# Kernel tuning notes

Hardware: AMD Instinct MI355X
Metric: run time of the kernel (lower is better)

Reference implementation:

```python
import jax, jax.numpy as jnp
import numpy as np

L = 8            # hash grid levels
T = 2 ** 19      # table size per level
F = 4            # feature dims per level
H = 64           # hidden features
BASE_RES, MAX_RES = 16.0, 1024.0
RES = jnp.asarray(BASE_RES * (MAX_RES / BASE_RES) ** (np.arange(L) / (L - 1)), dtype=jnp.float32)
PRIMES = jnp.array([1, 2654435761, 805459861], dtype=jnp.uint32)
CORNERS = jnp.array([[i >> 2 & 1, i >> 1 & 1, i & 1] for i in range(8)], dtype=jnp.float32)  # [8,3]
CORNERS_U = CORNERS.astype(jnp.uint32)


def hash_grid_encode(points, tables):
    # points: [N,3] in [0,1]; tables: [L,T,F] -> [N, L*F]
    def level(table, res):
        p = points * res                       # [N,3]
        p0 = jnp.floor(p)
        frac = p - p0                          # [N,3]
        idx0 = p0.astype(jnp.uint32)
        cidx = idx0[:, None, :] + CORNERS_U[None]          # [N,8,3]
        h = cidx * PRIMES                                   # uint32 wraparound
        h = (h[..., 0] ^ h[..., 1] ^ h[..., 2]) % jnp.uint32(T)
        feats = table[h.astype(jnp.int32)]                  # [N,8,F]
        w = jnp.prod(jnp.where(CORNERS[None] == 1.0, frac[:, None, :], 1.0 - frac[:, None, :]), axis=-1)  # [N,8]
        return jnp.sum(feats * w[..., None], axis=1)        # [N,F]
    out = jax.vmap(level, in_axes=(0, 0))(tables, RES)      # [L,N,F]
    return jnp.transpose(out, (1, 0, 2)).reshape(points.shape[0], L * F)


def sh4_encode(d):
    # 4th order (16-component) spherical harmonics of unit directions
    d = d / jnp.linalg.norm(d, axis=-1, keepdims=True)
    x, y, z = d[..., 0], d[..., 1], d[..., 2]
    xx, yy, zz = x * x, y * y, z * z
    return jnp.stack([
        jnp.full_like(x, 0.28209479177387814),
        -0.48860251190291987 * y,
        0.48860251190291987 * z,
        -0.48860251190291987 * x,
        1.0925484305920792 * x * y,
        -1.0925484305920792 * y * z,
        0.94617469575755997 * zz - 0.31539156525252005,
        -1.0925484305920792 * x * z,
        0.54627421529603959 * (xx - yy),
        -0.59004358992664352 * y * (3.0 * xx - yy),
        2.8906114426405538 * x * y * z,
        -0.45704579946446572 * y * (4.0 * zz - xx - yy),
        0.37317633259011546 * z * (2.0 * zz - 3.0 * xx - 3.0 * yy),
        -0.45704579946446572 * x * (4.0 * zz - xx - yy),
        1.4453057213202769 * z * (xx - yy),
        -0.59004358992664352 * x * (xx - 3.0 * yy),
    ], axis=-1)


def _dense(key, fan_in, fan_out):
    kw, kb = jax.random.split(key)
    W = jax.random.normal(kw, (fan_in, fan_out), jnp.float32) / jnp.sqrt(fan_in)
    b = jnp.zeros((fan_out,), jnp.float32)
    return W, b


def setup_inputs() -> dict:
    key = jax.random.key(0)
    ks = jax.random.split(key, 10)
    N = 524288
    input_points = jax.random.uniform(ks[0], (N, 3), jnp.float32)
    input_views = jax.random.normal(ks[1], (N, 3), jnp.float32)
    tables = jax.random.uniform(ks[2], (L, T, F), jnp.float32, -1e-4, 1e-4)
    W1, b1 = _dense(ks[3], L * F, H)
    W2, b2 = _dense(ks[4], H, H)
    W3, b3 = _dense(ks[5], H, 16)
    W4, b4 = _dense(ks[6], 15 + 16, H)
    W5, b5 = _dense(ks[7], H, H)
    W6, b6 = _dense(ks[8], H, H)
    W7, b7 = _dense(ks[9], H, 3)
    return dict(input_points=input_points, input_views=input_views, tables=tables,
                W1=W1, b1=b1, W2=W2, b2=b2, W3=W3, b3=b3, W4=W4, b4=b4,
                W5=W5, b5=b5, W6=W6, b6=b6, W7=W7, b7=b7)


def reference(input_points, input_views, tables, W1, b1, W2, b2, W3, b3, W4, b4, W5, b5, W6, b6, W7, b7):
    enc = hash_grid_encode(input_points, tables)       # [N,32]
    x = jax.nn.relu(enc @ W1 + b1)
    x = jax.nn.relu(x @ W2 + b2)
    x = x @ W3 + b3                                    # [N,16]
    densities = jax.nn.relu(x[..., 0])
    enc_dir = sh4_encode(input_views)                  # [N,16]
    x = jnp.concatenate([x[..., 1:], enc_dir], axis=-1)  # [N,31]
    x = jax.nn.relu(x @ W4 + b4)
    x = jax.nn.relu(x @ W5 + b5)
    x = jax.nn.relu(x @ W6 + b6)
    x = x @ W7 + b7                                    # [N,3]
    colors = jax.nn.sigmoid(x)
    return colors, densities
```

## Files before the change

### kernel.cpp

```cpp
#include <hip/hip_runtime.h>
#include <math.h>

#define TSZ (1u << 19)
#define TMASK (TSZ - 1u)

typedef __attribute__((ext_vector_type(8))) short bf8_t;
typedef __attribute__((ext_vector_type(4))) float f32x4;
typedef _Float16 h2_t __attribute__((ext_vector_type(2)));

struct ResArr { float r[8]; };
struct WPtrs { const float* w[7]; };

__device__ __forceinline__ unsigned short f2b(float x) {
    unsigned u = __float_as_uint(x);
    return (unsigned short)((u + 0x7fffu + ((u >> 16) & 1u)) >> 16);
}
__device__ __forceinline__ unsigned pack2(float a, float b) {
    return (unsigned)f2b(a) | ((unsigned)f2b(b) << 16);
}

__device__ __forceinline__ int swadr(int row, int e) {
    return row * 128 + ((((e >> 3) ^ (row & 7)) << 4)) + ((e & 7) << 1);
}

__device__ __forceinline__ unsigned enc8(float x) {
    float v = x * 1048576.0f;
    unsigned u = __float_as_uint(v);
    unsigned s = (u >> 24) & 0x80u;
    unsigned ua = u & 0x7fffffffu;
    unsigned r = ua + 0x7ffffu + ((ua >> 20) & 1u);
    int E = (int)(r >> 23) - 120;
    unsigned nrm = ((unsigned)E << 3) | ((r >> 20) & 7u);
    float t = __uint_as_float(ua) * 512.0f + 12582912.0f;
    unsigned den = __float_as_uint(t) & 0xfu;
    unsigned mag = (__uint_as_float(ua) >= 0.015625f) ? nrm : den;
    return s | mag;
}

__global__ void prep_all(const float4* __restrict__ tbl, uint4* __restrict__ tab_out,
                         WPtrs wp, unsigned short* __restrict__ wfrag) {
    int b = blockIdx.x;
    if (b < 4096) {
        int i = b * 256 + threadIdx.x;
        uint4 o;
        { float4 v = tbl[4 * i + 0]; o.x = enc8(v.x) | (enc8(v.y) << 8) | (enc8(v.z) << 16) | (enc8(v.w) << 24); }
        { float4 v = tbl[4 * i + 1]; o.y = enc8(v.x) | (enc8(v.y) << 8) | (enc8(v.z) << 16) | (enc8(v.w) << 24); }
        { float4 v = tbl[4 * i + 2]; o.z = enc8(v.x) | (enc8(v.y) << 8) | (enc8(v.z) << 16) | (enc8(v.w) << 24); }
        { float4 v = tbl[4 * i + 3]; o.w = enc8(v.x) | (enc8(v.y) << 8) | (enc8(v.z) << 16) | (enc8(v.w) << 24); }
        tab_out[i] = o;
        return;
    }
    int idx = (b - 4096) * 256 + threadIdx.x;
    if (idx >= 18432) return;
    int layer, base;
    if      (idx < 2048)  { layer = 0; base = 0;     }
    else if (idx < 6144)  { layer = 1; base = 2048;  }
    else if (idx < 7168)  { layer = 2; base = 6144;  }
    else if (idx < 9216)  { layer = 3; base = 7168;  }
    else if (idx < 13312) { layer = 4; base = 9216;  }
    else if (idx < 17408) { layer = 5; base = 13312; }
    else                  { layer = 6; base = 17408; }
    int rel  = idx - base;
    int frag = rel >> 9;
    int r    = rel & 511;
    int lane = r >> 3, j = r & 7;
    int quad = lane >> 4, col16 = lane & 15;
    int KS = (layer == 0 || layer == 3) ? 1 : 2;
    int nt = frag / KS, ks = frag % KS;
    int k = ks * 32 + quad * 8 + j;
    int n = nt * 16 + col16;
    int Kreal = (layer == 0) ? 32 : (layer == 3) ? 31 : 64;
    int Nw    = (layer == 2) ? 16 : (layer == 6) ? 3  : 64;
    float v = 0.0f;
    if (k < Kreal && n < Nw) v = wp.w[layer][k * Nw + n];
    wfrag[idx] = f2b(v);
}

__global__ void __launch_bounds__(256, 2) ngp_mfma(
    const float* __restrict__ pts, const float* __restrict__ views,
    const unsigned* __restrict__ tab8,
    const unsigned short* __restrict__ wfrag,
    const float* __restrict__ b1, const float* __restrict__ b2,
    const float* __restrict__ b3, const float* __restrict__ b4,
    const float* __restrict__ b5, const float* __restrict__ b6,
    const float* __restrict__ b7,
    ResArr res, float* __restrict__ out_col, float* __restrict__ out_den,
    int npts)
{
    __shared__ unsigned char act[4][8192];
    const int tid   = threadIdx.x;
    const int w     = tid >> 6;
    const int lane  = tid & 63;
    const int quad  = lane >> 4;
    const int col16 = lane & 15;
    unsigned char* actb = act[w];

    const int n0 = blockIdx.x * 256 + w * 64;
    if (n0 >= npts) return;
    int pt = n0 + lane;
    int ptc = pt < npts ? pt : npts - 1;

    const float px = pts[3 * ptc + 0];
    const float py = pts[3 * ptc + 1];
    const float pz = pts[3 * ptc + 2];
    float vx = views[3 * ptc + 0], vy = views[3 * ptc + 1], vz = views[3 * ptc + 2];

    uint2    gp[8][4];
    unsigned gs[8][4] = {};
    unsigned meta[8];
    float    tfr[8][3];
#pragma unroll
    for (int l = 0; l < 8; ++l) {
        float rr = res.r[l];
        float fx = px * rr, fy = py * rr, fz = pz * rr;
        float f0x = floorf(fx), f0y = floorf(fy), f0z = floorf(fz);
        unsigned ix = (unsigned)f0x, iy = (unsigned)f0y, iz = (unsigned)f0z;
        tfr[l][0] = fx - f0x; tfr[l][1] = fy - f0y; tfr[l][2] = fz - f0z;
        unsigned hy  = iy * 2654435761u,  hz  = iz * 805459861u;
        unsigned hy1 = hy + 2654435761u,  hz1 = hz + 805459861u;
        unsigned syz[4] = { hy ^ hz, hy ^ hz1, hy1 ^ hz, hy1 ^ hz1 };
        const unsigned* tl = tab8 + (size_t)l * TSZ;
        unsigned m = (ix & 1u) << 4;
#pragma unroll
        for (int c = 0; c < 4; ++c) {
            unsigned h0 = (ix ^ syz[c]) & TMASK;
            gp[l][c] = ((const uint2*)tl)[h0 >> 1];
            m |= (h0 & 1u) << c;
        }
        meta[l] = m;
        if (ix & 1u) {
            unsigned x1 = ix + 1u;
#pragma unroll
            for (int c = 0; c < 4; ++c) {
                unsigned h1 = (x1 ^ syz[c]) & TMASK;
                gs[l][c] = tl[h1];
            }
        }
    }

    float4 stash;
#pragma unroll
    for (int l = 0; l < 8; ++l) {
        float tx = tfr[l][0], ty = tfr[l][1], tz = tfr[l][2];
        float wx1 = tx, wx0 = 1.0f - tx;
        float wy1 = ty, wy0 = 1.0f - ty;
        float wz1 = tz, wz0 = 1.0f - tz;
        float wyz[4] = { wy0 * wz0, wy0 * wz1, wy1 * wz0, wy1 * wz1 };
        unsigned m = meta[l];
        h2_t acc01 = { (_Float16)0, (_Float16)0 };
        h2_t acc23 = { (_Float16)0, (_Float16)0 };
#pragma unroll
        for (int c = 0; c < 4; ++c) {
            uint2 pr = gp[l][c];
            bool hodd = (m >> c) & 1u;
            unsigned mine = hodd ? pr.y : pr.x;
            unsigned oth  = hodd ? pr.x : pr.y;
            unsigned nxt  = (m & 16u) ? gs[l][c] : oth;
#pragma unroll
            for (int half = 0; half < 2; ++half) {
                float wt = (half ? wx1 : wx0) * wyz[c];
                unsigned u = half ? nxt : mine;
                unsigned ws = (unsigned)__builtin_bit_cast(unsigned short, (_Float16)wt);
                h2_t w2 = __builtin_bit_cast(h2_t, __builtin_amdgcn_perm(0u, ws, 0x01000100u));
                unsigned p01 = __builtin_amdgcn_perm(0u, u, 0x01040004u);
                unsigned p23 = __builtin_amdgcn_perm(0u, u, 0x03040204u);
                unsigned m01 = (((p01 >> 1) & 0x3F803F80u) + 0x20002000u) | (p01 & 0x80008000u);
                unsigned m23 = (((p23 >> 1) & 0x3F803F80u) + 0x20002000u) | (p23 & 0x80008000u);
                acc01 = __builtin_bit_cast(h2_t, m01) * w2 + acc01;
                acc23 = __builtin_bit_cast(h2_t, m23) * w2 + acc23;
            }
        }
        const float SC = 9.5367431640625e-07f;
        float a0 = (float)acc01[0] * SC, a1 = (float)acc01[1] * SC;
        float a2 = (float)acc23[0] * SC, a3 = (float)acc23[1] * SC;
        if ((l & 1) == 0) {
            stash = make_float4(a0, a1, a2, a3);
        } else {
            uint4 pk;
            pk.x = pack2(stash.x, stash.y);
            pk.y = pack2(stash.z, stash.w);
            pk.z = pack2(a0, a1);
            pk.w = pack2(a2, a3);
            *(uint4*)(actb + lane * 128 + ((((l >> 1)) ^ (lane & 7)) << 4)) = pk;
        }
    }

    float inv = rsqrtf(vx * vx + vy * vy + vz * vz);
    vx *= inv; vy *= inv; vz *= inv;
    float xx = vx * vx, yy = vy * vy, zz = vz * vz;
    float sh[16];
    sh[0]  = 0.28209479177387814f;
    sh[1]  = -0.48860251190291987f * vy;
    sh[2]  = 0.48860251190291987f * vz;
    sh[3]  = -0.48860251190291987f * vx;
    sh[4]  = 1.0925484305920792f * vx * vy;
    sh[5]  = -1.0925484305920792f * vy * vz;
    sh[6]  = 0.94617469575755997f * zz - 0.31539156525252005f;
    sh[7]  = -1.0925484305920792f * vx * vz;
    sh[8]  = 0.54627421529603959f * (xx - yy);
    sh[9]  = -0.59004358992664352f * vy * (3.0f * xx - yy);
    sh[10] = 2.8906114426405538f * vx * vy * vz;
    sh[11] = -0.45704579946446572f * vy * (4.0f * zz - xx - yy);
    sh[12] = 0.37317633259011546f * vz * (2.0f * zz - 3.0f * xx - 3.0f * yy);
    sh[13] = -0.45704579946446572f * vx * (4.0f * zz - xx - yy);
    sh[14] = 1.4453057213202769f * vz * (xx - yy);
    sh[15] = -0.59004358992664352f * vx * (xx - 3.0f * yy);

#define LAYER_STD(KS, FB, BIAS)                                                          \
    {                                                                                    \
        bf8_t A[4][KS];                                                                  \
        _Pragma("unroll") for (int mt = 0; mt < 4; ++mt)                                 \
            _Pragma("unroll") for (int ks = 0; ks < KS; ++ks)                            \
                A[mt][ks] = *(const bf8_t*)(actb + swadr(mt * 16 + col16, ks * 32 + quad * 8)); \
        _Pragma("unroll") for (int nt = 0; nt < 4; ++nt) {                               \
            float bv = BIAS[nt * 16 + col16];                                            \
            f32x4 acc[4];                                                                \
            _Pragma("unroll") for (int mt = 0; mt < 4; ++mt) acc[mt] = f32x4{bv, bv, bv, bv}; \
            _Pragma("unroll") for (int ks = 0; ks < KS; ++ks) {                          \
                bf8_t B = ((const bf8_t*)(wfrag + FB + (nt * KS + ks) * 512))[lane];     \
                _Pragma("unroll") for (int mt = 0; mt < 4; ++mt)                         \
                    acc[mt] = __builtin_amdgcn_mfma_f32_16x16x32_bf16(A[mt][ks], B, acc[mt], 0, 0, 0); \
            }                                                                            \
            _Pragma("unroll") for (int mt = 0; mt < 4; ++mt)                             \
                _Pragma("unroll") for (int r = 0; r < 4; ++r) {                          \
                    int row = mt * 16 + quad * 4 + r;                                    \
                    *(unsigned short*)(actb + swadr(row, nt * 16 + col16)) =             \
                        f2b(fmaxf(acc[mt][r], 0.0f));                                    \
                }                                                                        \
        }                                                                                \
    }

    LAYER_STD(1, 0, b1)
    LAYER_STD(2, 2048, b2)

    {
        bf8_t A[4][2];
#pragma unroll
        for (int mt = 0; mt < 4; ++mt)
#pragma unroll
            for (int ks = 0; ks < 2; ++ks)
                A[mt][ks] = *(const bf8_t*)(actb + swadr(mt * 16 + col16, ks * 32 + quad * 8));
        float bv = b3[col16];
        f32x4 acc[4];
#pragma unroll
        for (int mt = 0; mt < 4; ++mt) acc[mt] = f32x4{bv, bv, bv, bv};
#pragma unroll
        for (int ks = 0; ks < 2; ++ks) {
            bf8_t B = ((const bf8_t*)(wfrag + 6144 + ks * 512))[lane];
#pragma unroll
            for (int mt = 0; mt < 4; ++mt)
                acc[mt] = __builtin_amdgcn_mfma_f32_16x16x32_bf16(A[mt][ks], B, acc[mt], 0, 0, 0);
        }
#pragma unroll
        for (int mt = 0; mt < 4; ++mt)
#pragma unroll
            for (int r = 0; r < 4; ++r) {
                int row = mt * 16 + quad * 4 + r;
                float v = acc[mt][r];
                if (col16 == 0) {
                    if (n0 + row < npts) out_den[n0 + row] = fmaxf(v, 0.0f);
                } else {
                    *(unsigned short*)(actb + swadr(row, col16 - 1)) = f2b(v);
                }
            }
    }

#pragma unroll
    for (int i = 0; i < 16; ++i)
        *(unsigned short*)(actb + swadr(lane, 15 + i)) = f2b(sh[i]);
    *(unsigned short*)(actb + swadr(lane, 31)) = 0;

    LAYER_STD(1, 7168, b4)
    LAYER_STD(2, 9216, b5)
    LAYER_STD(2, 13312, b6)

    {
        bf8_t A[4][2];
#pragma unroll
        for (int mt = 0; mt < 4; ++mt)
#pragma unroll
            for (int ks = 0; ks < 2; ++ks)
                A[mt][ks] = *(const bf8_t*)(actb + swadr(mt * 16 + col16, ks * 32 + quad * 8));
        float bv = (col16 < 3) ? b7[col16] : 0.0f;
        f32x4 acc[4];
#pragma unroll
        for (int mt = 0; mt < 4; ++mt) acc[mt] = f32x4{bv, bv, bv, bv};
#pragma unroll
        for (int ks = 0; ks < 2; ++ks) {
            bf8_t B = ((const bf8_t*)(wfrag + 17408 + ks * 512))[lane];
#pragma unroll
            for (int mt = 0; mt < 4; ++mt)
                acc[mt] = __builtin_amdgcn_mfma_f32_16x16x32_bf16(A[mt][ks], B, acc[mt], 0, 0, 0);
        }
        if (col16 < 3) {
#pragma unroll
            for (int mt = 0; mt < 4; ++mt)
#pragma unroll
                for (int r = 0; r < 4; ++r) {
                    int row = mt * 16 + quad * 4 + r;
                    if (n0 + row < npts) {
                        float s = 1.0f / (1.0f + expf(-acc[mt][r]));
                        out_col[(size_t)(n0 + row) * 3 + col16] = s;
                    }
                }
        }
    }
#undef LAYER_STD
}

extern "C" void kernel_launch(void* const* d_in, const int* in_sizes, int n_in,
                              void* d_out, int out_size, void* d_ws, size_t ws_size,
                              hipStream_t stream) {
    const float* pts    = (const float*)d_in[0];
    const float* views  = (const float*)d_in[1];
    const float* tables = (const float*)d_in[2];
    const float* W1 = (const float*)d_in[3];  const float* b1 = (const float*)d_in[4];
    const float* W2 = (const float*)d_in[5];  const float* b2 = (const float*)d_in[6];
    const float* W3 = (const float*)d_in[7];  const float* b3 = (const float*)d_in[8];
    const float* W4 = (const float*)d_in[9];  const float* b4 = (const float*)d_in[10];
    const float* W5 = (const float*)d_in[11]; const float* b5 = (const float*)d_in[12];
    const float* W6 = (const float*)d_in[13]; const float* b6 = (const float*)d_in[14];
    const float* W7 = (const float*)d_in[15]; const float* b7 = (const float*)d_in[16];

    const int N = in_sizes[0] / 3;
    float* out = (float*)d_out;
    float* out_col = out;
    float* out_den = out + (size_t)3 * N;

    unsigned* tab8        = (unsigned*)d_ws;
    unsigned short* wfrag = (unsigned short*)((char*)d_ws + (size_t)(TSZ) * 8 * 4);

    WPtrs wp;
    wp.w[0] = W1; wp.w[1] = W2; wp.w[2] = W3; wp.w[3] = W4;
    wp.w[4] = W5; wp.w[5] = W6; wp.w[6] = W7;
    prep_all<<<4096 + 72, 256, 0, stream>>>((const float4*)tables, (uint4*)tab8, wp, wfrag);

    ResArr res;
    for (int l = 0; l < 8; ++l)
        res.r[l] = (float)(16.0 * pow(64.0, (double)l / 7.0));

    const int grid = (N + 255) / 256;
    ngp_mfma<<<grid, 256, 0, stream>>>(pts, views, tab8, wfrag,
                                       b1, b2, b3, b4, b5, b6, b7,
                                       res, out_col, out_den, N);
}
```

Measured before the change: 291.9 us.

## Pipeline hash-grid gathers through a three-level rolling buffer and raise occupancy

Replaces the issue-all-eight-levels-then-combine gather scheme with a three-slot rolling pipeline: gathers for the next levels are issued while the current level is interpolated, and sched_barriers keep that order. This cuts the live register footprint of the gather buffers, which lets launch bounds ask for three blocks per SM instead of two. Spherical-harmonic computation is also moved to the point of use so its registers are not live during the gather phase. The trade-off is fewer gathers in flight per wave, offset by more resident waves, and the scheduling barriers may limit the compiler's freedom to interleave work.

```diff
diff --git a/kernel.cpp b/kernel.cpp
--- a/kernel.cpp
+++ b/kernel.cpp
@@ -76,7 +76,7 @@
     wfrag[idx] = f2b(v);
 }
 
-__global__ void __launch_bounds__(256, 2) ngp_mfma(
+__global__ void __launch_bounds__(256, 3) ngp_mfma(
     const float* __restrict__ pts, const float* __restrict__ views,
     const unsigned* __restrict__ tab8,
     const unsigned short* __restrict__ wfrag,
@@ -105,106 +105,99 @@
     const float pz = pts[3 * ptc + 2];
     float vx = views[3 * ptc + 0], vy = views[3 * ptc + 1], vz = views[3 * ptc + 2];
 
-    uint2    gp[8][4];
-    unsigned gs[8][4] = {};
-    unsigned meta[8];
-    float    tfr[8][3];
-#pragma unroll
-    for (int l = 0; l < 8; ++l) {
-        float rr = res.r[l];
-        float fx = px * rr, fy = py * rr, fz = pz * rr;
-        float f0x = floorf(fx), f0y = floorf(fy), f0z = floorf(fz);
-        unsigned ix = (unsigned)f0x, iy = (unsigned)f0y, iz = (unsigned)f0z;
-        tfr[l][0] = fx - f0x; tfr[l][1] = fy - f0y; tfr[l][2] = fz - f0z;
-        unsigned hy  = iy * 2654435761u,  hz  = iz * 805459861u;
-        unsigned hy1 = hy + 2654435761u,  hz1 = hz + 805459861u;
-        unsigned syz[4] = { hy ^ hz, hy ^ hz1, hy1 ^ hz, hy1 ^ hz1 };
-        const unsigned* tl = tab8 + (size_t)l * TSZ;
-        unsigned m = (ix & 1u) << 4;
-#pragma unroll
-        for (int c = 0; c < 4; ++c) {
-            unsigned h0 = (ix ^ syz[c]) & TMASK;
-            gp[l][c] = ((const uint2*)tl)[h0 >> 1];
-            m |= (h0 & 1u) << c;
-        }
-        meta[l] = m;
-        if (ix & 1u) {
-            unsigned x1 = ix + 1u;
-#pragma unroll
-            for (int c = 0; c < 4; ++c) {
-                unsigned h1 = (x1 ^ syz[c]) & TMASK;
-                gs[l][c] = tl[h1];
-            }
-        }
-    }
-
-    float4 stash;
-#pragma unroll
-    for (int l = 0; l < 8; ++l) {
-        float tx = tfr[l][0], ty = tfr[l][1], tz = tfr[l][2];
-        float wx1 = tx, wx0 = 1.0f - tx;
-        float wy1 = ty, wy0 = 1.0f - ty;
-        float wz1 = tz, wz0 = 1.0f - tz;
-        float wyz[4] = { wy0 * wz0, wy0 * wz1, wy1 * wz0, wy1 * wz1 };
-        unsigned m = meta[l];
-        h2_t acc01 = { (_Float16)0, (_Float16)0 };
-        h2_t acc23 = { (_Float16)0, (_Float16)0 };
-#pragma unroll
-        for (int c = 0; c < 4; ++c) {
-            uint2 pr = gp[l][c];
-            bool hodd = (m >> c) & 1u;
-            unsigned mine = hodd ? pr.y : pr.x;
-            unsigned oth  = hodd ? pr.x : pr.y;
-            unsigned nxt  = (m & 16u) ? gs[l][c] : oth;
-#pragma unroll
-            for (int half = 0; half < 2; ++half) {
-                float wt = (half ? wx1 : wx0) * wyz[c];
-                unsigned u = half ? nxt : mine;
-                unsigned ws = (unsigned)__builtin_bit_cast(unsigned short, (_Float16)wt);
-                h2_t w2 = __builtin_bit_cast(h2_t, __builtin_amdgcn_perm(0u, ws, 0x01000100u));
-                unsigned p01 = __builtin_amdgcn_perm(0u, u, 0x01040004u);
-                unsigned p23 = __builtin_amdgcn_perm(0u, u, 0x03040204u);
-                unsigned m01 = (((p01 >> 1) & 0x3F803F80u) + 0x20002000u) | (p01 & 0x80008000u);
-                unsigned m23 = (((p23 >> 1) & 0x3F803F80u) + 0x20002000u) | (p23 & 0x80008000u);
-                acc01 = __builtin_bit_cast(h2_t, m01) * w2 + acc01;
-                acc23 = __builtin_bit_cast(h2_t, m23) * w2 + acc23;
-            }
-        }
-        const float SC = 9.5367431640625e-07f;
-        float a0 = (float)acc01[0] * SC, a1 = (float)acc01[1] * SC;
-        float a2 = (float)acc23[0] * SC, a3 = (float)acc23[1] * SC;
-        if ((l & 1) == 0) {
-            stash = make_float4(a0, a1, a2, a3);
-        } else {
-            uint4 pk;
-            pk.x = pack2(stash.x, stash.y);
-            pk.y = pack2(stash.z, stash.w);
-            pk.z = pack2(a0, a1);
-            pk.w = pack2(a2, a3);
-            *(uint4*)(actb + lane * 128 + ((((l >> 1)) ^ (lane & 7)) << 4)) = pk;
-        }
-    }
-
-    float inv = rsqrtf(vx * vx + vy * vy + vz * vz);
-    vx *= inv; vy *= inv; vz *= inv;
-    float xx = vx * vx, yy = vy * vy, zz = vz * vz;
-    float sh[16];
-    sh[0]  = 0.28209479177387814f;
-    sh[1]  = -0.48860251190291987f * vy;
-    sh[2]  = 0.48860251190291987f * vz;
-    sh[3]  = -0.48860251190291987f * vx;
-    sh[4]  = 1.0925484305920792f * vx * vy;
-    sh[5]  = -1.0925484305920792f * vy * vz;
-    sh[6]  = 0.94617469575755997f * zz - 0.31539156525252005f;
-    sh[7]  = -1.0925484305920792f * vx * vz;
-    sh[8]  = 0.54627421529603959f * (xx - yy);
-    sh[9]  = -0.59004358992664352f * vy * (3.0f * xx - yy);
-    sh[10] = 2.8906114426405538f * vx * vy * vz;
-    sh[11] = -0.45704579946446572f * vy * (4.0f * zz - xx - yy);
-    sh[12] = 0.37317633259011546f * vz * (2.0f * zz - 3.0f * xx - 3.0f * yy);
-    sh[13] = -0.45704579946446572f * vx * (4.0f * zz - xx - yy);
-    sh[14] = 1.4453057213202769f * vz * (xx - yy);
-    sh[15] = -0.59004358992664352f * vx * (xx - 3.0f * yy);
+    uint2    gp[3][4];
+    unsigned gs[3][4];
+    unsigned meta[3];
+    float    tf[3][3];
+    float4   stash;
+
+#define GI(l, s) { \
+    float rr = res.r[l]; \
+    float fx = px * rr, fy = py * rr, fz = pz * rr; \
+    float f0x = floorf(fx), f0y = floorf(fy), f0z = floorf(fz); \
+    unsigned ix = (unsigned)f0x, iy = (unsigned)f0y, iz = (unsigned)f0z; \
+    tf[s][0] = fx - f0x; tf[s][1] = fy - f0y; tf[s][2] = fz - f0z; \
+    unsigned hy  = iy * 2654435761u,  hz  = iz * 805459861u; \
+    unsigned hy1 = hy + 2654435761u,  hz1 = hz + 805459861u; \
+    unsigned syz0 = hy ^ hz, syz1 = hy ^ hz1, syz2 = hy1 ^ hz, syz3 = hy1 ^ hz1; \
+    const unsigned* tl = tab8 + (size_t)(l) * TSZ; \
+    unsigned mm = (ix & 1u) << 4; \
+    { unsigned h0 = (ix ^ syz0) & TMASK; gp[s][0] = ((const uint2*)tl)[h0 >> 1]; mm |= (h0 & 1u); } \
+    { unsigned h0 = (ix ^ syz1) & TMASK; gp[s][1] = ((const uint2*)tl)[h0 >> 1]; mm |= (h0 & 1u) << 1; } \
+    { unsigned h0 = (ix ^ syz2) & TMASK; gp[s][2] = ((const uint2*)tl)[h0 >> 1]; mm |= (h0 & 1u) << 2; } \
+    { unsigned h0 = (ix ^ syz3) & TMASK; gp[s][3] = ((const uint2*)tl)[h0 >> 1]; mm |= (h0 & 1u) << 3; } \
+    meta[s] = mm; \
+    if (ix & 1u) { \
+        unsigned x1 = ix + 1u; \
+        gs[s][0] = tl[(x1 ^ syz0) & TMASK]; \
+        gs[s][1] = tl[(x1 ^ syz1) & TMASK]; \
+        gs[s][2] = tl[(x1 ^ syz2) & TMASK]; \
+        gs[s][3] = tl[(x1 ^ syz3) & TMASK]; \
+    } \
+}
+
+#define HALF(u_, wt_) { \
+    float wt = (wt_); unsigned u = (u_); \
+    unsigned ws = (unsigned)__builtin_bit_cast(unsigned short, (_Float16)wt); \
+    h2_t w2 = __builtin_bit_cast(h2_t, __builtin_amdgcn_perm(0u, ws, 0x01000100u)); \
+    unsigned p01 = __builtin_amdgcn_perm(0u, u, 0x01040004u); \
+    unsigned p23 = __builtin_amdgcn_perm(0u, u, 0x03040204u); \
+    unsigned m01 = (((p01 >> 1) & 0x3F803F80u) + 0x20002000u) | (p01 & 0x80008000u); \
+    unsigned m23 = (((p23 >> 1) & 0x3F803F80u) + 0x20002000u) | (p23 & 0x80008000u); \
+    acc01 = __builtin_bit_cast(h2_t, m01) * w2 + acc01; \
+    acc23 = __builtin_bit_cast(h2_t, m23) * w2 + acc23; \
+}
+
+#define CORNER(s, c, wyzc) { \
+    uint2 pr = gp[s][c]; \
+    bool hodd = (mc >> (c)) & 1u; \
+    unsigned mine = hodd ? pr.y : pr.x; \
+    unsigned oth  = hodd ? pr.x : pr.y; \
+    unsigned nxt  = (mc & 16u) ? gs[s][c] : oth; \
+    HALF(mine, wx0 * (wyzc)) \
+    HALF(nxt,  wx1 * (wyzc)) \
+}
+
+#define GC(l, s) { \
+    float tx = tf[s][0], ty = tf[s][1], tz = tf[s][2]; \
+    float wx1 = tx, wx0 = 1.0f - tx; \
+    float wy1 = ty, wy0 = 1.0f - ty; \
+    float wz1 = tz, wz0 = 1.0f - tz; \
+    float wyz0 = wy0 * wz0, wyz1 = wy0 * wz1, wyz2 = wy1 * wz0, wyz3 = wy1 * wz1; \
+    unsigned mc = meta[s]; \
+    h2_t acc01 = { (_Float16)0, (_Float16)0 }; \
+    h2_t acc23 = { (_Float16)0, (_Float16)0 }; \
+    CORNER(s, 0, wyz0) CORNER(s, 1, wyz1) CORNER(s, 2, wyz2) CORNER(s, 3, wyz3) \
+    const float SC = 9.5367431640625e-07f;   \
+    float a0 = (float)acc01[0] * SC, a1 = (float)acc01[1] * SC; \
+    float a2 = (float)acc23[0] * SC, a3 = (float)acc23[1] * SC; \
+    if (((l) & 1) == 0) { \
+        stash = make_float4(a0, a1, a2, a3); \
+    } else { \
+        uint4 pk_; \
+        pk_.x = pack2(stash.x, stash.y); \
+        pk_.y = pack2(stash.z, stash.w); \
+        pk_.z = pack2(a0, a1); \
+        pk_.w = pack2(a2, a3); \
+        *(uint4*)(actb + lane * 128 + (((((l) >> 1)) ^ (lane & 7)) << 4)) = pk_; \
+    } \
+}
+
+    GI(0, 0) GI(1, 1) GI(2, 2)
+    __builtin_amdgcn_sched_barrier(0);
+    GC(0, 0) GI(3, 0) __builtin_amdgcn_sched_barrier(0);
+    GC(1, 1) GI(4, 1) __builtin_amdgcn_sched_barrier(0);
+    GC(2, 2) GI(5, 2) __builtin_amdgcn_sched_barrier(0);
+    GC(3, 0) GI(6, 0) __builtin_amdgcn_sched_barrier(0);
+    GC(4, 1) GI(7, 1) __builtin_amdgcn_sched_barrier(0);
+    GC(5, 2)
+    GC(6, 0)
+    GC(7, 1)
+
+#undef GC
+#undef CORNER
+#undef HALF
+#undef GI
 
 #define LAYER_STD(KS, FB, BIAS)                                                          \
     {                                                                                    \
@@ -265,10 +258,33 @@
             }
     }
 
-#pragma unroll
-    for (int i = 0; i < 16; ++i)
-        *(unsigned short*)(actb + swadr(lane, 15 + i)) = f2b(sh[i]);
-    *(unsigned short*)(actb + swadr(lane, 31)) = 0;
+    {
+        float inv = rsqrtf(vx * vx + vy * vy + vz * vz);
+        vx *= inv; vy *= inv; vz *= inv;
+        float xx = vx * vx, yy = vy * vy, zz = vz * vz;
+        float sh[16];
+        sh[0]  = 0.28209479177387814f;
+        sh[1]  = -0.48860251190291987f * vy;
+        sh[2]  = 0.48860251190291987f * vz;
+        sh[3]  = -0.48860251190291987f * vx;
+        sh[4]  = 1.0925484305920792f * vx * vy;
+        sh[5]  = -1.0925484305920792f * vy * vz;
+        sh[6]  = 0.94617469575755997f * zz - 0.31539156525252005f;
+        sh[7]  = -1.0925484305920792f * vx * vz;
+        sh[8]  = 0.54627421529603959f * (xx - yy);
+        sh[9]  = -0.59004358992664352f * vy * (3.0f * xx - yy);
+        sh[10] = 2.8906114426405538f * vx * vy * vz;
+        sh[11] = -0.45704579946446572f * vy * (4.0f * zz - xx - yy);
+        sh[12] = 0.37317633259011546f * vz * (2.0f * zz - 3.0f * xx - 3.0f * yy);
+        sh[13] = -0.45704579946446572f * vx * (4.0f * zz - xx - yy);
+        sh[14] = 1.4453057213202769f * vz * (xx - yy);
+        sh[15] = -0.59004358992664352f * vx * (xx - 3.0f * yy);
+
+#pragma unroll
+        for (int i = 0; i < 16; ++i)
+            *(unsigned short*)(actb + swadr(lane, 15 + i)) = f2b(sh[i]);
+        *(unsigned short*)(actb + swadr(lane, 31)) = 0;
+    }
 
     LAYER_STD(1, 7168, b4)
     LAYER_STD(2, 9216, b5)
```

Measured after the change: 277.4 us. 1.05x faster.

## Split hash-grid gather into a separate per-level kernel before the MLP

Applied to the files above, without the earlier changes.

Splits the fused kernel in two. A new kernel runs one block per 256 points per level, gathers the table entries, trilerps them, and writes packed bf16 features to a workspace buffer. The MLP kernel then reads those features, computes the SH encoding later to shorten register live ranges, and runs at higher occupancy (launch bound raised from 2 to 4 blocks). This trades a global round trip for the encoding, plus an extra launch, for much lower register pressure and better latency hiding on the random gathers. Interleaving levels across blocks may also improve cache locality within each level's table.

```diff
diff --git a/kernel.cpp b/kernel.cpp
--- a/kernel.cpp
+++ b/kernel.cpp
@@ -35,6 +35,17 @@
     unsigned den = __float_as_uint(t) & 0xfu;
     unsigned mag = (__uint_as_float(ua) >= 0.015625f) ? nrm : den;
     return s | mag;
+}
+
+__device__ __forceinline__ void trilerp8(unsigned u, float wt, h2_t& acc01, h2_t& acc23) {
+    unsigned ws = (unsigned)__builtin_bit_cast(unsigned short, (_Float16)wt);
+    h2_t w2 = __builtin_bit_cast(h2_t, __builtin_amdgcn_perm(0u, ws, 0x01000100u));
+    unsigned p01 = __builtin_amdgcn_perm(0u, u, 0x01040004u);
+    unsigned p23 = __builtin_amdgcn_perm(0u, u, 0x03040204u);
+    unsigned m01 = (((p01 >> 1) & 0x3F803F80u) + 0x20002000u) | (p01 & 0x80008000u);
+    unsigned m23 = (((p23 >> 1) & 0x3F803F80u) + 0x20002000u) | (p23 & 0x80008000u);
+    acc01 = __builtin_bit_cast(h2_t, m01) * w2 + acc01;
+    acc23 = __builtin_bit_cast(h2_t, m23) * w2 + acc23;
 }
 
 __global__ void prep_all(const float4* __restrict__ tbl, uint4* __restrict__ tab_out,
@@ -76,15 +87,78 @@
     wfrag[idx] = f2b(v);
 }
 
-__global__ void __launch_bounds__(256, 2) ngp_mfma(
-    const float* __restrict__ pts, const float* __restrict__ views,
-    const unsigned* __restrict__ tab8,
+__global__ void __launch_bounds__(256, 8) hash_gather(
+    const float* __restrict__ pts, const unsigned* __restrict__ tab8,
+    uint2* __restrict__ enc, ResArr res, int npts)
+{
+    const int bid = blockIdx.x;
+    const int l   = bid & 7;
+    const int i   = (bid >> 3) * 256 + threadIdx.x;
+    if (i >= npts) return;
+
+    const float px = pts[3 * i + 0];
+    const float py = pts[3 * i + 1];
+    const float pz = pts[3 * i + 2];
+
+    const float rr = res.r[l];
+    float fx = px * rr, fy = py * rr, fz = pz * rr;
+    float f0x = floorf(fx), f0y = floorf(fy), f0z = floorf(fz);
+    unsigned ix = (unsigned)f0x, iy = (unsigned)f0y, iz = (unsigned)f0z;
+    float tx = fx - f0x, ty = fy - f0y, tz = fz - f0z;
+
+    unsigned hy  = iy * 2654435761u,  hz  = iz * 805459861u;
+    unsigned hy1 = hy + 2654435761u,  hz1 = hz + 805459861u;
+    unsigned syz[4] = { hy ^ hz, hy ^ hz1, hy1 ^ hz, hy1 ^ hz1 };
+    const unsigned* tl = tab8 + (size_t)l * TSZ;
+
+    uint2    gp[4];
+    unsigned gs[4] = {};
+    unsigned mm = (ix & 1u) << 4;
+#pragma unroll
+    for (int c = 0; c < 4; ++c) {
+        unsigned h0 = (ix ^ syz[c]) & TMASK;
+        gp[c] = ((const uint2*)tl)[h0 >> 1];
+        mm |= (h0 & 1u) << c;
+    }
+    if (ix & 1u) {
+        unsigned x1 = ix + 1u;
+#pragma unroll
+        for (int c = 0; c < 4; ++c) gs[c] = tl[(x1 ^ syz[c]) & TMASK];
+    }
+
+    float wx1 = tx, wx0 = 1.0f - tx;
+    float wy1 = ty, wy0 = 1.0f - ty;
+    float wz1 = tz, wz0 = 1.0f - tz;
+    float wyz[4] = { wy0 * wz0, wy0 * wz1, wy1 * wz0, wy1 * wz1 };
+
+    h2_t acc01 = { (_Float16)0, (_Float16)0 };
+    h2_t acc23 = { (_Float16)0, (_Float16)0 };
+#pragma unroll
+    for (int c = 0; c < 4; ++c) {
+        uint2 pr = gp[c];
+        bool hodd = (mm >> c) & 1u;
+        unsigned mine = hodd ? pr.y : pr.x;
+        unsigned oth  = hodd ? pr.x : pr.y;
+        unsigned nxt  = (mm & 16u) ? gs[c] : oth;
+        trilerp8(mine, wx0 * wyz[c], acc01, acc23);
+        trilerp8(nxt,  wx1 * wyz[c], acc01, acc23);
+    }
+    const float SC = 9.5367431640625e-07f;
+    float a0 = (float)acc01[0] * SC, a1 = (float)acc01[1] * SC;
+    float a2 = (float)acc23[0] * SC, a3 = (float)acc23[1] * SC;
+    uint2 o; o.x = pack2(a0, a1); o.y = pack2(a2, a3);
+    enc[(size_t)l * npts + i] = o;
+}
+
+__global__ void __launch_bounds__(256, 4) ngp_mlp(
+    const float* __restrict__ views,
+    const uint2* __restrict__ enc,
     const unsigned short* __restrict__ wfrag,
     const float* __restrict__ b1, const float* __restrict__ b2,
     const float* __restrict__ b3, const float* __restrict__ b4,
     const float* __restrict__ b5, const float* __restrict__ b6,
     const float* __restrict__ b7,
-    ResArr res, float* __restrict__ out_col, float* __restrict__ out_den,
+    float* __restrict__ out_col, float* __restrict__ out_den,
     int npts)
 {
     __shared__ unsigned char act[4][8192];
@@ -100,111 +174,16 @@
     int pt = n0 + lane;
     int ptc = pt < npts ? pt : npts - 1;
 
-    const float px = pts[3 * ptc + 0];
-    const float py = pts[3 * ptc + 1];
-    const float pz = pts[3 * ptc + 2];
     float vx = views[3 * ptc + 0], vy = views[3 * ptc + 1], vz = views[3 * ptc + 2];
 
-    uint2    gp[8][4];
-    unsigned gs[8][4] = {};
-    unsigned meta[8];
-    float    tfr[8][3];
-#pragma unroll
-    for (int l = 0; l < 8; ++l) {
-        float rr = res.r[l];
-        float fx = px * rr, fy = py * rr, fz = pz * rr;
-        float f0x = floorf(fx), f0y = floorf(fy), f0z = floorf(fz);
-        unsigned ix = (unsigned)f0x, iy = (unsigned)f0y, iz = (unsigned)f0z;
-        tfr[l][0] = fx - f0x; tfr[l][1] = fy - f0y; tfr[l][2] = fz - f0z;
-        unsigned hy  = iy * 2654435761u,  hz  = iz * 805459861u;
-        unsigned hy1 = hy + 2654435761u,  hz1 = hz + 805459861u;
-        unsigned syz[4] = { hy ^ hz, hy ^ hz1, hy1 ^ hz, hy1 ^ hz1 };
-        const unsigned* tl = tab8 + (size_t)l * TSZ;
-        unsigned m = (ix & 1u) << 4;
-#pragma unroll
-        for (int c = 0; c < 4; ++c) {
-            unsigned h0 = (ix ^ syz[c]) & TMASK;
-            gp[l][c] = ((const uint2*)tl)[h0 >> 1];
-            m |= (h0 & 1u) << c;
-        }
-        meta[l] = m;
-        if (ix & 1u) {
-            unsigned x1 = ix + 1u;
-#pragma unroll
-            for (int c = 0; c < 4; ++c) {
-                unsigned h1 = (x1 ^ syz[c]) & TMASK;
-                gs[l][c] = tl[h1];
-            }
-        }
-    }
-
-    float4 stash;
-#pragma unroll
-    for (int l = 0; l < 8; ++l) {
-        float tx = tfr[l][0], ty = tfr[l][1], tz = tfr[l][2];
-        float wx1 = tx, wx0 = 1.0f - tx;
-        float wy1 = ty, wy0 = 1.0f - ty;
-        float wz1 = tz, wz0 = 1.0f - tz;
-        float wyz[4] = { wy0 * wz0, wy0 * wz1, wy1 * wz0, wy1 * wz1 };
-        unsigned m = meta[l];
-        h2_t acc01 = { (_Float16)0, (_Float16)0 };
-        h2_t acc23 = { (_Float16)0, (_Float16)0 };
-#pragma unroll
-        for (int c = 0; c < 4; ++c) {
-            uint2 pr = gp[l][c];
-            bool hodd = (m >> c) & 1u;
-            unsigned mine = hodd ? pr.y : pr.x;
-            unsigned oth  = hodd ? pr.x : pr.y;
-            unsigned nxt  = (m & 16u) ? gs[l][c] : oth;
-#pragma unroll
-            for (int half = 0; half < 2; ++half) {
-                float wt = (half ? wx1 : wx0) * wyz[c];
-                unsigned u = half ? nxt : mine;
-                unsigned ws = (unsigned)__builtin_bit_cast(unsigned short, (_Float16)wt);
-                h2_t w2 = __builtin_bit_cast(h2_t, __builtin_amdgcn_perm(0u, ws, 0x01000100u));
-                unsigned p01 = __builtin_amdgcn_perm(0u, u, 0x01040004u);
-                unsigned p23 = __builtin_amdgcn_perm(0u, u, 0x03040204u);
-                unsigned m01 = (((p01 >> 1) & 0x3F803F80u) + 0x20002000u) | (p01 & 0x80008000u);
-                unsigned m23 = (((p23 >> 1) & 0x3F803F80u) + 0x20002000u) | (p23 & 0x80008000u);
-                acc01 = __builtin_bit_cast(h2_t, m01) * w2 + acc01;
-                acc23 = __builtin_bit_cast(h2_t, m23) * w2 + acc23;
-            }
-        }
-        const float SC = 9.5367431640625e-07f;
-        float a0 = (float)acc01[0] * SC, a1 = (float)acc01[1] * SC;
-        float a2 = (float)acc23[0] * SC, a3 = (float)acc23[1] * SC;
-        if ((l & 1) == 0) {
-            stash = make_float4(a0, a1, a2, a3);
-        } else {
-            uint4 pk;
-            pk.x = pack2(stash.x, stash.y);
-            pk.y = pack2(stash.z, stash.w);
-            pk.z = pack2(a0, a1);
-            pk.w = pack2(a2, a3);
-            *(uint4*)(actb + lane * 128 + ((((l >> 1)) ^ (lane & 7)) << 4)) = pk;
-        }
-    }
-
-    float inv = rsqrtf(vx * vx + vy * vy + vz * vz);
-    vx *= inv; vy *= inv; vz *= inv;
-    float xx = vx * vx, yy = vy * vy, zz = vz * vz;
-    float sh[16];
-    sh[0]  = 0.28209479177387814f;
-    sh[1]  = -0.48860251190291987f * vy;
-    sh[2]  = 0.48860251190291987f * vz;
-    sh[3]  = -0.48860251190291987f * vx;
-    sh[4]  = 1.0925484305920792f * vx * vy;
-    sh[5]  = -1.0925484305920792f * vy * vz;
-    sh[6]  = 0.94617469575755997f * zz - 0.31539156525252005f;
-    sh[7]  = -1.0925484305920792f * vx * vz;
-    sh[8]  = 0.54627421529603959f * (xx - yy);
-    sh[9]  = -0.59004358992664352f * vy * (3.0f * xx - yy);
-    sh[10] = 2.8906114426405538f * vx * vy * vz;
-    sh[11] = -0.45704579946446572f * vy * (4.0f * zz - xx - yy);
-    sh[12] = 0.37317633259011546f * vz * (2.0f * zz - 3.0f * xx - 3.0f * yy);
-    sh[13] = -0.45704579946446572f * vx * (4.0f * zz - xx - yy);
-    sh[14] = 1.4453057213202769f * vz * (xx - yy);
-    sh[15] = -0.59004358992664352f * vx * (xx - 3.0f * yy);
+#pragma unroll
+    for (int lp = 0; lp < 4; ++lp) {
+        uint2 e0 = enc[(size_t)(2 * lp + 0) * npts + ptc];
+        uint2 e1 = enc[(size_t)(2 * lp + 1) * npts + ptc];
+        uint4 pk;
+        pk.x = e0.x; pk.y = e0.y; pk.z = e1.x; pk.w = e1.y;
+        *(uint4*)(actb + lane * 128 + ((lp ^ (lane & 7)) << 4)) = pk;
+    }
 
 #define LAYER_STD(KS, FB, BIAS)                                                          \
     {                                                                                    \
@@ -265,10 +244,33 @@
             }
     }
 
-#pragma unroll
-    for (int i = 0; i < 16; ++i)
-        *(unsigned short*)(actb + swadr(lane, 15 + i)) = f2b(sh[i]);
-    *(unsigned short*)(actb + swadr(lane, 31)) = 0;
+    {
+        float inv = rsqrtf(vx * vx + vy * vy + vz * vz);
+        vx *= inv; vy *= inv; vz *= inv;
+        float xx = vx * vx, yy = vy * vy, zz = vz * vz;
+        float sh[16];
+        sh[0]  = 0.28209479177387814f;
+        sh[1]  = -0.48860251190291987f * vy;
+        sh[2]  = 0.48860251190291987f * vz;
+        sh[3]  = -0.48860251190291987f * vx;
+        sh[4]  = 1.0925484305920792f * vx * vy;
+        sh[5]  = -1.0925484305920792f * vy * vz;
+        sh[6]  = 0.94617469575755997f * zz - 0.31539156525252005f;
+        sh[7]  = -1.0925484305920792f * vx * vz;
+        sh[8]  = 0.54627421529603959f * (xx - yy);
+        sh[9]  = -0.59004358992664352f * vy * (3.0f * xx - yy);
+        sh[10] = 2.8906114426405538f * vx * vy * vz;
+        sh[11] = -0.45704579946446572f * vy * (4.0f * zz - xx - yy);
+        sh[12] = 0.37317633259011546f * vz * (2.0f * zz - 3.0f * xx - 3.0f * yy);
+        sh[13] = -0.45704579946446572f * vx * (4.0f * zz - xx - yy);
+        sh[14] = 1.4453057213202769f * vz * (xx - yy);
+        sh[15] = -0.59004358992664352f * vx * (xx - 3.0f * yy);
+
+#pragma unroll
+        for (int i = 0; i < 16; ++i)
+            *(unsigned short*)(actb + swadr(lane, 15 + i)) = f2b(sh[i]);
+        *(unsigned short*)(actb + swadr(lane, 31)) = 0;
+    }
 
     LAYER_STD(1, 7168, b4)
     LAYER_STD(2, 9216, b5)
@@ -329,6 +331,7 @@
 
     unsigned* tab8        = (unsigned*)d_ws;
     unsigned short* wfrag = (unsigned short*)((char*)d_ws + (size_t)(TSZ) * 8 * 4);
+    uint2* enc            = (uint2*)((char*)d_ws + (size_t)17 * 1024 * 1024);
 
     WPtrs wp;
     wp.w[0] = W1; wp.w[1] = W2; wp.w[2] = W3; wp.w[3] = W4;
@@ -339,8 +342,9 @@
     for (int l = 0; l < 8; ++l)
         res.r[l] = (float)(16.0 * pow(64.0, (double)l / 7.0));
 
-    const int grid = (N + 255) / 256;
-    ngp_mfma<<<grid, 256, 0, stream>>>(pts, views, tab8, wfrag,
-                                       b1, b2, b3, b4, b5, b6, b7,
-                                       res, out_col, out_den, N);
-}
+    const int chunks = (N + 255) / 256;
+    hash_gather<<<chunks * 8, 256, 0, stream>>>(pts, tab8, enc, res, N);
+    ngp_mlp<<<chunks, 256, 0, stream>>>(views, enc, wfrag,
+                                        b1, b2, b3, b4, b5, b6, b7,
+                                        out_col, out_den, N);
+}
```

New measurement: 369.9 us. 26.7% more time.
